# Optimization experiments

Hardware: AMD Instinct MI355X
Metric: run time of the kernel (lower is better)

The kernel has to match this reference:

```python
import jax, jax.numpy as jnp
import numpy as np
from jax import lax

BN_EPS = 1e-5
SQ_EPS = 1e-8


def squash(s, axis=-1):
    # v = (|s|^2 / (1+|s|^2)) * s / |s|
    n2 = jnp.sum(s * s, axis=axis, keepdims=True)
    return (n2 / (1.0 + n2)) * s / jnp.sqrt(n2 + SQ_EPS)


def setup_inputs() -> dict:
    key = jax.random.key(0)
    ks = jax.random.split(key, 5)
    B, C, H, W = 64, 512, 28, 28
    NUM_ROUTES = 8 * 10 * 10  # lower_num_caps * 10 * 10 after k9 s2 conv on 28x28
    features = jax.random.normal(ks[0], (B, C, H, W), jnp.float32)
    conv1_w = jax.random.normal(ks[1], (256, 512, 3, 3), jnp.float32) * 0.02
    conv1_b = jnp.zeros((256,), jnp.float32)
    bn_gamma = jnp.ones((256,), jnp.float32)
    bn_beta = jnp.zeros((256,), jnp.float32)
    bn_mean = jnp.zeros((256,), jnp.float32)
    bn_var = jnp.ones((256,), jnp.float32)
    prim_w = jax.random.normal(ks[2], (256, 256, 9, 9), jnp.float32) * 0.02
    prim_b = jnp.zeros((256,), jnp.float32)
    # routing transform: (num_routes, higher_num_caps, out_dim, in_dim)
    route_w = jax.random.normal(ks[3], (NUM_ROUTES, 2, 16, 32), jnp.float32) * 0.05
    return {"features": features, "conv1_w": conv1_w, "conv1_b": conv1_b,
            "bn_gamma": bn_gamma, "bn_beta": bn_beta, "bn_mean": bn_mean,
            "bn_var": bn_var, "prim_w": prim_w, "prim_b": prim_b,
            "route_w": route_w}


def reference(features, conv1_w, conv1_b, bn_gamma, bn_beta, bn_mean, bn_var,
              prim_w, prim_b, route_w):
    B = features.shape[0]
    dn = ("NCHW", "OIHW", "NCHW")
    # pre_conv: Conv2d(512->256, k3, pad1) + BatchNorm (eval) + ReLU
    x = lax.conv_general_dilated(features, conv1_w, (1, 1), "SAME",
                                 dimension_numbers=dn)
    x = x + conv1_b[None, :, None, None]
    inv = bn_gamma * lax.rsqrt(bn_var + BN_EPS)
    x = x * inv[None, :, None, None] + (bn_beta - bn_mean * inv)[None, :, None, None]
    x = jax.nn.relu(x)
    # primary capsules: Conv2d(256->8*32, k9, s2, valid) -> (B,256,10,10)
    p = lax.conv_general_dilated(x, prim_w, (2, 2), "VALID",
                                 dimension_numbers=dn)
    p = p + prim_b[None, :, None, None]
    Hp, Wp = p.shape[2], p.shape[3]
    # (B, num_caps, cap_dim, Hp*Wp) -> (B, num_caps*Hp*Wp, cap_dim)
    p = p.reshape(B, 8, 32, Hp * Wp).transpose(0, 1, 3, 2).reshape(B, 8 * Hp * Wp, 32)
    lower_caps = squash(p, axis=-1)  # (B, 800, 32)
    # predictions u_hat: (B, routes, higher_caps, out_dim)
    u_hat = jnp.einsum("bri,rjoi->brjo", lower_caps, route_w)
    # dynamic routing-by-agreement
    b = jnp.zeros((B, u_hat.shape[1], u_hat.shape[2]), u_hat.dtype)
    n_iter = 3
    for it in range(n_iter):
        c = jax.nn.softmax(b, axis=2)                  # coupling coeffs
        s = jnp.einsum("brj,brjo->bjo", c, u_hat)      # weighted sum
        v = squash(s, axis=-1)                          # (B, 2, 16)
        if it < n_iter - 1:
            b = b + jnp.einsum("brjo,bjo->brj", u_hat, v)
    return (lower_caps, v)
```

## Files before the change

kernel.cpp:

```cpp
#include <hip/hip_runtime.h>
#include <hip/hip_bf16.h>

#define BN_EPS 1e-5f
#define SQ_EPS 1e-8f

typedef __hip_bfloat16 bf16;
typedef __attribute__((ext_vector_type(8))) short bf16x8;
typedef __attribute__((ext_vector_type(4))) float f32x4;

__device__ __forceinline__ void gload_lds16(const void* g, void* l) {
    __builtin_amdgcn_global_load_lds(
        (const __attribute__((address_space(1))) unsigned int*)g,
        (__attribute__((address_space(3))) unsigned int*)l, 16, 0, 0);
}

__device__ __forceinline__ unsigned short f2bfu(float f) {
    bf16 h = __float2bfloat16(f);
    return *(unsigned short*)&h;
}

__global__ __launch_bounds__(256) void feat_to_nhwc(
    const float* __restrict__ feat, bf16* __restrict__ featP) {
    int b = blockIdx.z, ct = blockIdx.y, pt = blockIdx.x;
    int ci0 = ct * 64, px0 = pt * 64;
    int tid = threadIdx.x;
    __shared__ float t[64][65];
#pragma unroll
    for (int rep = 0; rep < 16; rep++) {
        int ci_l = rep * 4 + (tid >> 6);
        int px = px0 + (tid & 63);
        float v = 0.f;
        if (px < 784) v = feat[(b * 512 + ci0 + ci_l) * 784 + px];
        t[ci_l][tid & 63] = v;
    }
    __syncthreads();
#pragma unroll
    for (int rep = 0; rep < 4; rep++) {
        int px_l = rep * 16 + (tid >> 4);
        int px = px0 + px_l;
        if (px < 784) {
            int h = px / 28, wq = px % 28;
            int ci = (tid & 15) * 4;
            ushort4 o;
            o.x = f2bfu(t[ci + 0][px_l]);
            o.y = f2bfu(t[ci + 1][px_l]);
            o.z = f2bfu(t[ci + 2][px_l]);
            o.w = f2bfu(t[ci + 3][px_l]);
            *(ushort4*)&featP[((b * 30 + h + 1) * 30 + (wq + 1)) * 512 + ci0 + ci] = o;
        }
    }
}

__global__ __launch_bounds__(256) void wF_transform(
    const float* __restrict__ w1, const float* __restrict__ w2,
    bf16* __restrict__ wt1F, bf16* __restrict__ wt2F,
    bf16* __restrict__ featP) {
    __shared__ float tt[10368];
    if (blockIdx.x >= 768) {
        int b = blockIdx.x - 768;
        uint4 zz = {0u, 0u, 0u, 0u};
        for (int i = threadIdx.x; i < 116 * 64; i += 256) {
            int rp = i >> 6;
            int ci = (i & 63) * 8;
            int hp, wp;
            if (rp < 30)      { hp = 0;       wp = rp; }
            else if (rp < 60) { hp = 29;      wp = rp - 30; }
            else if (rp < 88) { hp = rp - 59; wp = 0; }
            else              { hp = rp - 87; wp = 29; }
            *(uint4*)&featP[(b * 900 + hp * 30 + wp) * 512 + ci] = zz;
        }
        return;
    }
    if (blockIdx.x < 256) {
        int co = blockIdx.x;
        const float* src = w1 + co * 4608;
        for (int i = threadIdx.x; i < 4608; i += 256) tt[i] = src[i];
        __syncthreads();
        int co16 = co >> 4, l15 = co & 15;
        for (int i = threadIdx.x; i < 576; i += 256) {
            int g = i >> 6, cc = (i >> 2) & 15, kq = i & 3;
            short v[8];
#pragma unroll
            for (int j = 0; j < 8; j++) {
                unsigned short u = f2bfu(tt[(cc * 32 + kq * 8 + j) * 9 + g]);
                v[j] = (short)u;
            }
            int fidx = cc * 9 + g;
            bf16x8* dst = (bf16x8*)&wt1F[(fidx * 16 + co16) * 512 + (kq * 16 + l15) * 8];
            bf16x8 pk = {v[0], v[1], v[2], v[3], v[4], v[5], v[6], v[7]};
            *dst = pk;
        }
    } else {
        int bid = blockIdx.x - 256;
        int half = bid & 1, co = bid >> 1;
        const float* src = w2 + co * 20736 + half * 10368;
        for (int i = threadIdx.x; i < 10368; i += 256) tt[i] = src[i];
        __syncthreads();
        int co16 = co >> 4, l15 = co & 15;
        for (int i = threadIdx.x; i < 1296; i += 256) {
            int sh = i >> 4, ccl = (i >> 2) & 3, kq = i & 3;
            int z = sh / 10; if (z > 7) z = 7;
            int s0 = (81 * z) >> 3;
            int ns = ((81 * (z + 1)) >> 3) - s0;
            int fidx = s0 * 8 + (half * 4 + ccl) * ns + (sh - s0);
            short v[8];
#pragma unroll
            for (int j = 0; j < 8; j++) {
                unsigned short u = f2bfu(tt[(ccl * 32 + kq * 8 + j) * 81 + sh]);
                v[j] = (short)u;
            }
            bf16x8* dst = (bf16x8*)&wt2F[(fidx * 16 + co16) * 512 + (kq * 16 + l15) * 8];
            bf16x8 pk = {v[0], v[1], v[2], v[3], v[4], v[5], v[6], v[7]};
            *dst = pk;
        }
    }
}

__global__ __launch_bounds__(512, 4) void conv1_mfma(
    const bf16* __restrict__ featP, const bf16* __restrict__ wt1F,
    const float* __restrict__ bias, const float* __restrict__ gamma,
    const float* __restrict__ beta, const float* __restrict__ mean,
    const float* __restrict__ var, bf16* __restrict__ x) {
    __shared__ char As4[4 * 7168];
    const int tid = threadIdx.x, lane = tid & 63, w = tid >> 6;
    const int Mt = blockIdx.x;

    const bf16* pA0;
    {
        int r0 = (w << 4) + (lane >> 2);
        int q = (lane & 3) ^ ((r0 >> 1) & 3);
        int m0 = Mt * 112 + (w < 7 ? r0 : 0);
        int b0 = m0 / 784, rr = m0 % 784, h0 = rr / 28, w0 = rr % 28;
        pA0 = featP + ((b0 * 30 + h0) * 30 + w0) * 512 + q * 8;
    }
    const bf16x8* pB = (const bf16x8*)wt1F + w * 128 + lane;

    int a_off[7];
#pragma unroll
    for (int mi = 0; mi < 7; mi++) {
        int r = mi * 16 + (lane & 15);
        a_off[mi] = r * 64 + (((lane >> 4) ^ ((r >> 1) & 3)) * 16);
    }

    f32x4 acc[7][2];
#pragma unroll
    for (int i = 0; i < 7; i++)
#pragma unroll
        for (int j = 0; j < 2; j++) acc[i][j] = f32x4{0.f, 0.f, 0.f, 0.f};

    bf16x8 Bv0[2], Bv1[2];

#define STG1(bi, offE)                                                     \
    do {                                                                   \
        if (w < 7)                                                         \
            gload_lds16(pA0 + (offE), As4 + (bi) * 7168 + w * 1024);       \
    } while (0)

    STG1(0, 0); STG1(1, 512); STG1(2, 1024);
    { const bf16x8* bp = pB; Bv0[0] = bp[0]; Bv0[1] = bp[64]; }
    asm volatile("s_waitcnt vmcnt(2)" ::: "memory");
    __builtin_amdgcn_s_barrier();
    asm volatile("" ::: "memory");

#define C1_STEP(u, BU, BL)                                                 \
    do {                                                                   \
        const int t_ = t + (u);                                            \
        int ttc = t_ + 3; if (ttc > 143) ttc = 143;                        \
        {       \
            int cc_ = ttc / 9, g_ = ttc - 9 * cc_;                         \
            int ky_ = g_ / 3, kx_ = g_ - 3 * ky_;                          \
            STG1((u + 3) & 3, (ky_ * 30 + kx_) * 512 + cc_ * 32);          \
        }                                                                  \
        {                                                                  \
            int fn = t_ + 1; if (fn > 143) fn = 143;                       \
            const bf16x8* bp = pB + fn * 1024;                             \
            BL[0] = bp[0]; BL[1] = bp[64];                                 \
        }                                                                  \
        const char* Ab = As4 + (u) * 7168;                                 \
        bf16x8 af[7];                                                      \
        _Pragma("unroll")                                                  \
        for (int mi = 0; mi < 7; mi++)                                     \
            af[mi] = *(const bf16x8*)(Ab + a_off[mi]);                     \
        __builtin_amdgcn_s_setprio(1);                                     \
        _Pragma("unroll")                                                  \
        for (int nj = 0; nj < 2; nj++)                                     \
            _Pragma("unroll")                                              \
            for (int mi = 0; mi < 7; mi++)                                 \
                acc[mi][nj] = __builtin_amdgcn_mfma_f32_16x16x32_bf16(     \
                    af[mi], BU[nj], acc[mi][nj], 0, 0, 0);                 \
        __builtin_amdgcn_s_setprio(0);                                     \
        if (t_ < 143) {                                                    \
            asm volatile("s_waitcnt vmcnt(8)" ::: "memory");               \
            __builtin_amdgcn_s_barrier();                                  \
            asm volatile("" ::: "memory");                                 \
        }                                                                  \
    } while (0)

    for (int t = 0; t < 144; t += 4) {
        C1_STEP(0, Bv0, Bv1);
        C1_STEP(1, Bv1, Bv0);
        C1_STEP(2, Bv0, Bv1);
        C1_STEP(3, Bv1, Bv0);
    }

#pragma unroll
    for (int nj = 0; nj < 2; nj++) {
        int co = w * 32 + nj * 16 + (lane & 15);
        float inv = gamma[co] * rsqrtf(var[co] + BN_EPS);
        float sh = beta[co] - mean[co] * inv;
        float bs = bias[co];
#pragma unroll
        for (int mi = 0; mi < 7; mi++) {
            int m0 = Mt * 112 + mi * 16 + ((lane >> 4) << 2);
#pragma unroll
            for (int r = 0; r < 4; r++) {
                float v = (acc[mi][nj][r] + bs) * inv + sh;
                x[(m0 + r) * 256 + co] = __float2bfloat16(fmaxf(v, 0.f));
            }
        }
    }
#undef STG1
#undef C1_STEP
}

__global__ __launch_bounds__(512, 4) void conv2_mfma(
    const bf16* __restrict__ x, const bf16* __restrict__ wt2F,
    bf16* __restrict__ p_parts) {
    __shared__ char As4[4 * 8192];
    const int tid = threadIdx.x, lane = tid & 63, w = tid >> 6;
    const int z = blockIdx.x & 7, Mt = blockIdx.x >> 3;
    const int sh0 = (81 * z) >> 3, sh1 = (81 * (z + 1)) >> 3;
    const int nsh = sh1 - sh0;
    const int NT = nsh << 3;
    const int FB = sh0 << 3;

    const bf16* pA0;
    {
        int r0 = (w << 4) + (lane >> 2);
        int q = (lane & 3) ^ ((r0 >> 1) & 3);
        int m0 = Mt * 128 + r0;
        int b0 = m0 / 100, s0 = m0 % 100, ho0 = s0 / 10, wo0 = s0 % 10;
        pA0 = x + ((b0 * 28 + 2 * ho0) * 28 + 2 * wo0) * 256 + q * 8;
    }
    const bf16x8* pB = (const bf16x8*)wt2F + w * 128 + lane;

    int a_off[8];
#pragma unroll
    for (int mi = 0; mi < 8; mi++) {
        int r = mi * 16 + (lane & 15);
        a_off[mi] = r * 64 + (((lane >> 4) ^ ((r >> 1) & 3)) * 16);
    }

    f32x4 acc[8][2];
#pragma unroll
    for (int i = 0; i < 8; i++)
#pragma unroll
        for (int j = 0; j < 2; j++) acc[i][j] = f32x4{0.f, 0.f, 0.f, 0.f};

    bf16x8 Bv0[2], Bv1[2];

#define STG2(bi, offE)                                                     \
    gload_lds16(pA0 + (offE), As4 + (bi) * 8192 + w * 1024)

#define A2OFF(tt)                                                          \
    ({ int ttc_ = (tt) < NT ? (tt) : NT - 1;                               \
       int cc_ = ttc_ / nsh, si_ = ttc_ - cc_ * nsh;                       \
       int sh_ = sh0 + si_;                                                \
       int ky_ = sh_ / 9, kx_ = sh_ - 9 * ky_;                             \
       (ky_ * 28 + kx_) * 256 + cc_ * 32; })

    STG2(0, A2OFF(0)); STG2(1, A2OFF(1)); STG2(2, A2OFF(2));
    { const bf16x8* bp = pB + FB * 1024; Bv0[0] = bp[0]; Bv0[1] = bp[64]; }
    asm volatile("s_waitcnt vmcnt(2)" ::: "memory");
    __builtin_amdgcn_s_barrier();
    asm volatile("" ::: "memory");

#define C2_STEP(u, BU, BL)                                                 \
    do {                                                                   \
        const int t_ = t + (u);                                            \
        STG2((u + 3) & 3, A2OFF(t_ + 3));                                  \
        {                                                                  \
            int fn = t_ + 1; if (fn > NT - 1) fn = NT - 1;                 \
            const bf16x8* bp = pB + (FB + fn) * 1024;                      \
            BL[0] = bp[0]; BL[1] = bp[64];                                 \
        }                                                                  \
        const char* Ab = As4 + (u) * 8192;                                 \
        bf16x8 af[8];                                                      \
        _Pragma("unroll")                                                  \
        for (int mi = 0; mi < 8; mi++)                                     \
            af[mi] = *(const bf16x8*)(Ab + a_off[mi]);                     \
        __builtin_amdgcn_s_setprio(1);                                     \
        _Pragma("unroll")                                                  \
        for (int nj = 0; nj < 2; nj++)                                     \
            _Pragma("unroll")                                              \
            for (int mi = 0; mi < 8; mi++)                                 \
                acc[mi][nj] = __builtin_amdgcn_mfma_f32_16x16x32_bf16(     \
                    af[mi], BU[nj], acc[mi][nj], 0, 0, 0);                 \
        __builtin_amdgcn_s_setprio(0);                                     \
        if (t_ < NT - 1) {                                                 \
            asm volatile("s_waitcnt vmcnt(8)" ::: "memory");               \
            __builtin_amdgcn_s_barrier();                                  \
            asm volatile("" ::: "memory");                                 \
        }                                                                  \
    } while (0)

    for (int t = 0; t < NT; t += 4) {
        C2_STEP(0, Bv0, Bv1);
        C2_STEP(1, Bv1, Bv0);
        C2_STEP(2, Bv0, Bv1);
        C2_STEP(3, Bv1, Bv0);
    }

#pragma unroll
    for (int nj = 0; nj < 2; nj++) {
        int co = w * 32 + nj * 16 + (lane & 15);
#pragma unroll
        for (int mi = 0; mi < 8; mi++) {
            int m0 = Mt * 128 + mi * 16 + ((lane >> 4) << 2);
#pragma unroll
            for (int r = 0; r < 4; r++)
                p_parts[(z * 6400 + m0 + r) * 256 + co] =
                    __float2bfloat16(acc[mi][nj][r]);
        }
    }
#undef STG2
#undef A2OFF
#undef C2_STEP
}

__global__ __launch_bounds__(256) void squash_kernel(
    const bf16* __restrict__ pp, const float* __restrict__ pb,
    float* __restrict__ lc) {
    int rowg = blockIdx.x * 8 + (threadIdx.x >> 5);
    int i = threadIdx.x & 31;
    int b = rowg / 800, r = rowg - b * 800;
    int cap = r / 100, s = r - cap * 100;
    int m = b * 100 + s, co = cap * 32 + i;
    float val = pb[co];
#pragma unroll
    for (int zz = 0; zz < 8; zz++)
        val += __bfloat162float(pp[(zz * 6400 + m) * 256 + co]);
    float n2 = val * val;
#pragma unroll
    for (int msk = 1; msk < 32; msk <<= 1) n2 += __shfl_xor(n2, msk);
    float scale = n2 / ((1.f + n2) * sqrtf(n2 + SQ_EPS));
    lc[(b * 800 + r) * 32 + i] = val * scale;
}

__global__ __launch_bounds__(256) void uhat_kernel(
    const float* __restrict__ lc, const float* __restrict__ rw,
    bf16* __restrict__ uht) {
    int rT = blockIdx.x, bT = blockIdx.y;
    int rl = threadIdx.x >> 5, jo = threadIdx.x & 31;
    int r = rT * 8 + rl;
    float4 wreg[8];
    const float4* wp4 = reinterpret_cast<const float4*>(rw + (r * 32 + jo) * 32);
#pragma unroll
    for (int k = 0; k < 8; k++) wreg[k] = wp4[k];
    for (int b = bT * 16; b < bT * 16 + 16; b++) {
        const float4* lp4 = reinterpret_cast<const float4*>(lc + (b * 800 + r) * 32);
        float acc = 0.f;
#pragma unroll
        for (int k = 0; k < 8; k++) {
            float4 a = lp4[k];
            acc = fmaf(a.x, wreg[k].x, acc);
            acc = fmaf(a.y, wreg[k].y, acc);
            acc = fmaf(a.z, wreg[k].z, acc);
            acc = fmaf(a.w, wreg[k].w, acc);
        }
        uht[(b * 32 + jo) * 800 + r] = __float2bfloat16(acc);
    }
}

__global__ __launch_bounds__(256) void route_all(
    const bf16* __restrict__ uht, float* __restrict__ vout) {
    extern __shared__ float rs[];
    float* u = rs;
    float* lg = rs + 26400;
    float* red = lg + 1600;
    float* vs = red + 256;
    int b = blockIdx.x, tid = threadIdx.x;
    for (int i = tid; i < 25600; i += 256) {
        int jo = i / 800, r = i - jo * 800;
        u[r * 33 + jo] = __bfloat162float(uht[(b * 32 + jo) * 800 + r]);
    }
    for (int i = tid; i < 1600; i += 256) lg[i] = 0.f;
    __syncthreads();
    int jo = tid & 31, rg = tid >> 5;
    for (int it = 0; it < 3; it++) {
        float sp = 0.f;
        for (int r = rg; r < 800; r += 8) {
            float l0 = lg[r * 2], l1 = lg[r * 2 + 1];
            float m = fmaxf(l0, l1);
            float e0 = __expf(l0 - m), e1 = __expf(l1 - m);
            float c = ((jo < 16) ? e0 : e1) / (e0 + e1);
            sp += c * u[r * 33 + jo];
        }
        red[rg * 32 + jo] = sp;
        __syncthreads();
        if (tid < 32) {
            float s = 0.f;
#pragma unroll
            for (int k = 0; k < 8; k++) s += red[k * 32 + tid];
            float n2 = s * s;
#pragma unroll
            for (int m = 1; m < 16; m <<= 1) n2 += __shfl_xor(n2, m);
            float scale = n2 / ((1.f + n2) * sqrtf(n2 + SQ_EPS));
            float v = s * scale;
            vs[tid] = v;
            if (it == 2) vout[b * 32 + tid] = v;
        }
        __syncthreads();
        if (it < 2) {
            for (int r = tid; r < 800; r += 256) {
                float d0 = 0.f, d1 = 0.f;
#pragma unroll
                for (int o = 0; o < 16; o++) {
                    d0 += u[r * 33 + o] * vs[o];
                    d1 += u[r * 33 + 16 + o] * vs[16 + o];
                }
                lg[r * 2] += d0;
                lg[r * 2 + 1] += d1;
            }
            __syncthreads();
        }
    }
}

extern "C" void kernel_launch(void* const* d_in, const int* in_sizes, int n_in,
                              void* d_out, int out_size, void* d_ws, size_t ws_size,
                              hipStream_t stream) {
    const float* feat    = (const float*)d_in[0];
    const float* conv1_w = (const float*)d_in[1];
    const float* conv1_b = (const float*)d_in[2];
    const float* bn_g    = (const float*)d_in[3];
    const float* bn_b    = (const float*)d_in[4];
    const float* bn_m    = (const float*)d_in[5];
    const float* bn_v    = (const float*)d_in[6];
    const float* prim_w  = (const float*)d_in[7];
    const float* prim_b  = (const float*)d_in[8];
    const float* route_w = (const float*)d_in[9];
    float* out = (float*)d_out;

    char* wsb = (char*)d_ws;
    bf16*  featP   = (bf16*)(wsb + 0);
    bf16*  p_parts = (bf16*)(wsb + 0);
    bf16*  uht     = (bf16*)(wsb + 26214400);
    bf16*  x       = (bf16*)(wsb + 58982400);
    bf16*  wt1F    = (bf16*)(wsb + 84672512);
    bf16*  wt2F    = (bf16*)(wsb + 87031808);

    float* lc_out = out;
    float* v_out  = out + 64 * 800 * 32;

    hipFuncSetAttribute((const void*)route_all,
                        hipFuncAttributeMaxDynamicSharedMemorySize, 113152);

    feat_to_nhwc<<<dim3(13, 8, 64), 256, 0, stream>>>(feat, featP);
    wF_transform<<<832, 256, 0, stream>>>(conv1_w, prim_w, wt1F, wt2F, featP);

    conv1_mfma<<<448, 512, 0, stream>>>(
        featP, wt1F, conv1_b, bn_g, bn_b, bn_m, bn_v, x);

    conv2_mfma<<<400, 512, 0, stream>>>(x, wt2F, p_parts);

    squash_kernel<<<6400, 256, 0, stream>>>(p_parts, prim_b, lc_out);

    uhat_kernel<<<dim3(100, 4), 256, 0, stream>>>(lc_out, route_w, uht);

    route_all<<<64, 256, 113152, stream>>>(uht, v_out);
}
```

Measured before the change: 300.0 us.

## Tile conv2 per batch image and fuse squash into u_hat kernel

conv2 now assigns one batch image (100 output pixels) per M tile, using 7 row fragments instead of 8 and padding the rows past 100. The grid grows to 512 blocks, which drops the cross-image index math but wastes about 12% of the MFMA work on padded rows. The split-K partial sums are stored interleaved, so the 8 partials for each element form one contiguous 16-byte vector. The separate squash kernel is folded into the u_hat kernel: it sums the partials, squashes, and writes lower_caps, then reuses the values through shared memory. This removes a launch and a global round trip of lower_caps.

```diff
diff --git a/kernel.cpp b/kernel.cpp
--- a/kernel.cpp
+++ b/kernel.cpp
@@ -17,6 +17,12 @@
 __device__ __forceinline__ unsigned short f2bfu(float f) {
     bf16 h = __float2bfloat16(f);
     return *(unsigned short*)&h;
+}
+
+__device__ __forceinline__ float bfu2f(short s) {
+    unsigned short u = (unsigned short)s;
+    bf16 h = *(bf16*)&u;
+    return __bfloat162float(h);
 }
 
 __global__ __launch_bounds__(256) void feat_to_nhwc(
@@ -166,7 +172,7 @@
     do {                                                                   \
         const int t_ = t + (u);                                            \
         int ttc = t_ + 3; if (ttc > 143) ttc = 143;                        \
-        {       \
+        {                                                                  \
             int cc_ = ttc / 9, g_ = ttc - 9 * cc_;                         \
             int ky_ = g_ / 3, kx_ = g_ - 3 * ky_;                          \
             STG1((u + 3) & 3, (ky_ * 30 + kx_) * 512 + cc_ * 32);          \
@@ -226,7 +232,7 @@
 __global__ __launch_bounds__(512, 4) void conv2_mfma(
     const bf16* __restrict__ x, const bf16* __restrict__ wt2F,
     bf16* __restrict__ p_parts) {
-    __shared__ char As4[4 * 8192];
+    __shared__ char As4[4 * 7168];
     const int tid = threadIdx.x, lane = tid & 63, w = tid >> 6;
     const int z = blockIdx.x & 7, Mt = blockIdx.x >> 3;
     const int sh0 = (81 * z) >> 3, sh1 = (81 * (z + 1)) >> 3;
@@ -237,30 +243,34 @@
     const bf16* pA0;
     {
         int r0 = (w << 4) + (lane >> 2);
-        int q = (lane & 3) ^ ((r0 >> 1) & 3);
-        int m0 = Mt * 128 + r0;
-        int b0 = m0 / 100, s0 = m0 % 100, ho0 = s0 / 10, wo0 = s0 % 10;
-        pA0 = x + ((b0 * 28 + 2 * ho0) * 28 + 2 * wo0) * 256 + q * 8;
+        int rr = (w < 7) ? r0 : 0;
+        int s = rr < 100 ? rr : 99;
+        int q = (lane & 3) ^ ((rr >> 1) & 3);
+        int ho = s / 10, wo = s - ho * 10;
+        pA0 = x + ((Mt * 28 + 2 * ho) * 28 + 2 * wo) * 256 + q * 8;
     }
     const bf16x8* pB = (const bf16x8*)wt2F + w * 128 + lane;
 
-    int a_off[8];
-#pragma unroll
-    for (int mi = 0; mi < 8; mi++) {
+    int a_off[7];
+#pragma unroll
+    for (int mi = 0; mi < 7; mi++) {
         int r = mi * 16 + (lane & 15);
         a_off[mi] = r * 64 + (((lane >> 4) ^ ((r >> 1) & 3)) * 16);
     }
 
-    f32x4 acc[8][2];
-#pragma unroll
-    for (int i = 0; i < 8; i++)
+    f32x4 acc[7][2];
+#pragma unroll
+    for (int i = 0; i < 7; i++)
 #pragma unroll
         for (int j = 0; j < 2; j++) acc[i][j] = f32x4{0.f, 0.f, 0.f, 0.f};
 
     bf16x8 Bv0[2], Bv1[2];
 
 #define STG2(bi, offE)                                                     \
-    gload_lds16(pA0 + (offE), As4 + (bi) * 8192 + w * 1024)
+    do {                                                                   \
+        if (w < 7)                                                         \
+            gload_lds16(pA0 + (offE), As4 + (bi) * 7168 + w * 1024);       \
+    } while (0)
 
 #define A2OFF(tt)                                                          \
     ({ int ttc_ = (tt) < NT ? (tt) : NT - 1;                               \
@@ -284,16 +294,16 @@
             const bf16x8* bp = pB + (FB + fn) * 1024;                      \
             BL[0] = bp[0]; BL[1] = bp[64];                                 \
         }                                                                  \
-        const char* Ab = As4 + (u) * 8192;                                 \
-        bf16x8 af[8];                                                      \
+        const char* Ab = As4 + (u) * 7168;                                 \
+        bf16x8 af[7];                                                      \
         _Pragma("unroll")                                                  \
-        for (int mi = 0; mi < 8; mi++)                                     \
+        for (int mi = 0; mi < 7; mi++)                                     \
             af[mi] = *(const bf16x8*)(Ab + a_off[mi]);                     \
         __builtin_amdgcn_s_setprio(1);                                     \
         _Pragma("unroll")                                                  \
         for (int nj = 0; nj < 2; nj++)                                     \
             _Pragma("unroll")                                              \
-            for (int mi = 0; mi < 8; mi++)                                 \
+            for (int mi = 0; mi < 7; mi++)                                 \
                 acc[mi][nj] = __builtin_amdgcn_mfma_f32_16x16x32_bf16(     \
                     af[mi], BU[nj], acc[mi][nj], 0, 0, 0);                 \
         __builtin_amdgcn_s_setprio(0);                                     \
@@ -315,12 +325,15 @@
     for (int nj = 0; nj < 2; nj++) {
         int co = w * 32 + nj * 16 + (lane & 15);
 #pragma unroll
-        for (int mi = 0; mi < 8; mi++) {
-            int m0 = Mt * 128 + mi * 16 + ((lane >> 4) << 2);
-#pragma unroll
-            for (int r = 0; r < 4; r++)
-                p_parts[(z * 6400 + m0 + r) * 256 + co] =
-                    __float2bfloat16(acc[mi][nj][r]);
+        for (int mi = 0; mi < 7; mi++) {
+            int row0 = mi * 16 + ((lane >> 4) << 2);
+#pragma unroll
+            for (int r = 0; r < 4; r++) {
+                int row = row0 + r;
+                if (row < 100)
+                    p_parts[((Mt * 100 + row) * 256 + co) * 8 + z] =
+                        __float2bfloat16(acc[mi][nj][r]);
+            }
         }
     }
 #undef STG2
@@ -328,41 +341,38 @@
 #undef C2_STEP
 }
 
-__global__ __launch_bounds__(256) void squash_kernel(
+__global__ __launch_bounds__(256) void squash_uhat(
     const bf16* __restrict__ pp, const float* __restrict__ pb,
-    float* __restrict__ lc) {
-    int rowg = blockIdx.x * 8 + (threadIdx.x >> 5);
-    int i = threadIdx.x & 31;
-    int b = rowg / 800, r = rowg - b * 800;
-    int cap = r / 100, s = r - cap * 100;
-    int m = b * 100 + s, co = cap * 32 + i;
-    float val = pb[co];
-#pragma unroll
-    for (int zz = 0; zz < 8; zz++)
-        val += __bfloat162float(pp[(zz * 6400 + m) * 256 + co]);
-    float n2 = val * val;
-#pragma unroll
-    for (int msk = 1; msk < 32; msk <<= 1) n2 += __shfl_xor(n2, msk);
-    float scale = n2 / ((1.f + n2) * sqrtf(n2 + SQ_EPS));
-    lc[(b * 800 + r) * 32 + i] = val * scale;
-}
-
-__global__ __launch_bounds__(256) void uhat_kernel(
-    const float* __restrict__ lc, const float* __restrict__ rw,
+    const float* __restrict__ rw, float* __restrict__ lc,
     bf16* __restrict__ uht) {
     int rT = blockIdx.x, bT = blockIdx.y;
     int rl = threadIdx.x >> 5, jo = threadIdx.x & 31;
     int r = rT * 8 + rl;
     float4 wreg[8];
-    const float4* wp4 = reinterpret_cast<const float4*>(rw + (r * 32 + jo) * 32);
+    const float4* wp4 = (const float4*)(rw + (r * 32 + jo) * 32);
 #pragma unroll
     for (int k = 0; k < 8; k++) wreg[k] = wp4[k];
+    int cap = r / 100, s = r - cap * 100;
+    int co = cap * 32 + jo;
+    float bsv = pb[co];
+    __shared__ float vrow[8][32];
     for (int b = bT * 16; b < bT * 16 + 16; b++) {
-        const float4* lp4 = reinterpret_cast<const float4*>(lc + (b * 800 + r) * 32);
+        int m = b * 100 + s;
+        bf16x8 pk = *(const bf16x8*)&pp[(m * 256 + co) * 8];
+        float val = bsv;
+#pragma unroll
+        for (int j = 0; j < 8; j++) val += bfu2f(pk[j]);
+        float n2 = val * val;
+#pragma unroll
+        for (int msk = 1; msk < 32; msk <<= 1) n2 += __shfl_xor(n2, msk);
+        float scale = n2 / ((1.f + n2) * sqrtf(n2 + SQ_EPS));
+        float sval = val * scale;
+        lc[(b * 800 + r) * 32 + jo] = sval;
+        vrow[rl][jo] = sval;
         float acc = 0.f;
 #pragma unroll
         for (int k = 0; k < 8; k++) {
-            float4 a = lp4[k];
+            float4 a = *(const float4*)&vrow[rl][k * 4];
             acc = fmaf(a.x, wreg[k].x, acc);
             acc = fmaf(a.y, wreg[k].y, acc);
             acc = fmaf(a.z, wreg[k].z, acc);
@@ -462,11 +472,10 @@
     conv1_mfma<<<448, 512, 0, stream>>>(
         featP, wt1F, conv1_b, bn_g, bn_b, bn_m, bn_v, x);
 
-    conv2_mfma<<<400, 512, 0, stream>>>(x, wt2F, p_parts);
-
-    squash_kernel<<<6400, 256, 0, stream>>>(p_parts, prim_b, lc_out);
-
-    uhat_kernel<<<dim3(100, 4), 256, 0, stream>>>(lc_out, route_w, uht);
+    conv2_mfma<<<512, 512, 0, stream>>>(x, wt2F, p_parts);
+
+    squash_uhat<<<dim3(100, 4), 256, 0, stream>>>(
+        p_parts, prim_b, route_w, lc_out, uht);
 
     route_all<<<64, 256, 113152, stream>>>(uht, v_out);
 }
```

Result: slower. 317.8 us (+5.9%).
